# Performance work log

Measured on AMD Instinct MI355X. Metric: run time of the kernel, lower is better.

The kernel has to match this reference:

```python
import jax, jax.numpy as jnp
import numpy as np

ENC_H = 512
DEC_H = 1024

def setup_inputs() -> dict:
    key = jax.random.key(0)
    k1, k2, k3, k4 = jax.random.split(key, 4)
    B, S = 32, 2048
    s = jax.random.normal(k1, (B, DEC_H), dtype=jnp.float32)
    encoder_outputs = jax.random.normal(k2, (B, S, 2 * ENC_H), dtype=jnp.float32)
    # nn.Linear weights: attn: [dec_h, 2*enc_h + dec_h], v: [1, dec_h]
    fan_in_attn = 2 * ENC_H + DEC_H
    attn_w = jax.random.uniform(k3, (DEC_H, fan_in_attn), dtype=jnp.float32,
                                minval=-1.0, maxval=1.0) / np.sqrt(fan_in_attn)
    v_w = jax.random.uniform(k4, (1, DEC_H), dtype=jnp.float32,
                             minval=-1.0, maxval=1.0) / np.sqrt(DEC_H)
    return {"s": s, "encoder_outputs": encoder_outputs, "attn_w": attn_w, "v_w": v_w}

def reference(s, encoder_outputs, attn_w, v_w):
    # Split attn weight to avoid materializing the repeated/concatenated tensor:
    # cat([s_rep, enc], -1) @ W^T == s @ Ws^T (broadcast over S) + enc @ We^T
    W_s = attn_w[:, :DEC_H]            # [dec_h, dec_h] acts on s
    W_e = attn_w[:, DEC_H:]            # [dec_h, 2*enc_h] acts on encoder_outputs
    proj_s = jnp.einsum('bd,hd->bh', s, W_s)                   # [B, dec_h]
    proj_e = jnp.einsum('bse,he->bsh', encoder_outputs, W_e)   # [B, S, dec_h]
    energy = jnp.tanh(proj_s[:, None, :] + proj_e)             # [B, S, dec_h]
    scores = jnp.einsum('bsh,oh->bs', energy, v_w)             # [B, S]
    return jax.nn.softmax(scores, axis=1)
```

## Files before the change

kernel.cpp:

```cpp
#include <hip/hip_runtime.h>
#include <hip/hip_bf16.h>

#define KDIM 1024
#define HDIM 1024
#define BM   64
#define SPART 65536

typedef __attribute__((ext_vector_type(8))) short bf16x8_t;
typedef __attribute__((ext_vector_type(16))) float f32x16_t;
typedef __attribute__((ext_vector_type(4))) float f32x4_t;
typedef __attribute__((ext_vector_type(4))) unsigned int u32x4_t;
typedef __attribute__((ext_vector_type(2))) unsigned int u32x2_t;

#define WAITVM(n) asm volatile("s_waitcnt vmcnt(" #n ")" ::: "memory")
#define MEMFENCE() asm volatile("" ::: "memory")

__device__ __forceinline__ unsigned int pack2bf(float a, float b) {
    union { float f; unsigned int u; } ua, ub;
    ua.f = a; ub.f = b;
    unsigned int ra = (ua.u + 0x7fffu + ((ua.u >> 16) & 1u)) >> 16;
    unsigned int rb = (ub.u + 0x7fffu + ((ub.u >> 16) & 1u)) >> 16;
    return ra | (rb << 16);
}

__device__ __forceinline__ unsigned int cvtpk(float lo, float hi) {
    unsigned int r;
    asm("v_cvt_pk_bf16_f32 %0, %1, %2" : "=v"(r) : "v"(lo), "v"(hi));
    return r;
}

__device__ __forceinline__ void gload16(const void* g, void* l) {
    __builtin_amdgcn_global_load_lds(
        (const __attribute__((address_space(1))) void*)g,
        (__attribute__((address_space(3))) void*)l, 16, 0, 0);
}

__global__ void cvt_we_k(const float* __restrict__ attn_w, unsigned short* __restrict__ we_t) {
    const int h = blockIdx.x;
    const int t = threadIdx.x;
    const f32x4_t v = *(const f32x4_t*)(attn_w + (size_t)h * 2048 + 1024 + (size_t)t * 4);
    u32x2_t o;
    o[0] = pack2bf(v[0], v[1]);
    o[1] = pack2bf(v[2], v[3]);
    const int ks  = t >> 2;
    const int e15 = (t & 3) * 4;
    *(u32x2_t*)&we_t[(size_t)ks * 16384 + h * 16 + e15] = o;
}

__global__ void proj_s_k(const float* __restrict__ s, const float* __restrict__ attn_w,
                         float* __restrict__ ps) {
    const int h = (blockIdx.x * blockDim.x + threadIdx.x) >> 6;
    const int lane = threadIdx.x & 63;
    const float* wr = attn_w + (size_t)h * 2048;
    float w[16];
#pragma unroll
    for (int i = 0; i < 16; ++i) w[i] = wr[lane + 64 * i];
    for (int b = 0; b < 32; ++b) {
        const float* sr = s + (size_t)b * 1024;
        float a = 0.f;
#pragma unroll
        for (int i = 0; i < 16; ++i) a = fmaf(w[i], sr[lane + 64 * i], a);
#pragma unroll
        for (int off = 32; off >= 1; off >>= 1) a += __shfl_xor(a, off, 64);
        if (lane == 0) ps[b * 1024 + h] = a;
    }
}

__launch_bounds__(512, 4)
__global__ void fused_main3_k(const float* __restrict__ enc,
                              const unsigned short* __restrict__ we_t,
                              const float* __restrict__ ps,
                              const float* __restrict__ vw,
                              float* __restrict__ scores_part) {
    __shared__ float lds_a[4 * 64 * 64];

    const int t = threadIdx.x;
    const int bid = blockIdx.x;
    const int xcd   = bid & 7;
    const int hhalf = (bid >> 3) & 1;
    const int m_swz = xcd * 128 + (bid >> 4);
    const int m_base = m_swz * BM;
    const int bidx = m_swz >> 5;

    const int lane = t & 63;
    const int wid  = t >> 6;
    const int l31  = lane & 31;
    const int h5   = lane >> 5;
    const int habs = hhalf * 512 + wid * 64;

    const int gr = t >> 4;
    const int gc = (t & 15) ^ (gr & 15);
    const float* gbase0 = enc + (size_t)(m_base + gr) * KDIM + gc * 4;
    const float* gbase1 = gbase0 + (size_t)32 * KDIM;

    auto stageG = [&](int kc) {
        const float* g0 = gbase0 + kc * 64;
        const float* g1 = gbase1 + kc * 64;
        char* d = (char*)lds_a + (kc & 3) * 16384 + t * 16;
        gload16(g0, d);
        gload16(g1, d + 8192);
    };

    const unsigned short* btile = we_t + (size_t)(habs + l31) * 16 + h5 * 8;
    auto loadB = [&](int g, bf16x8_t* dst) {
        const unsigned short* bp = btile + (size_t)g * 16384;
        dst[0] = *(const bf16x8_t*)(bp);
        dst[1] = *(const bf16x8_t*)(bp + 512);
    };

    f32x16_t acc[2][2];
#pragma unroll
    for (int m = 0; m < 2; ++m)
#pragma unroll
        for (int nf = 0; nf < 2; ++nf)
#pragma unroll
            for (int r = 0; r < 16; ++r) acc[m][nf][r] = 0.f;

    bf16x8_t bbuf[4][2];

    stageG(0);
    stageG(1);
    MEMFENCE();
    loadB(0, bbuf[0]);
    loadB(1, bbuf[1]);
    loadB(2, bbuf[2]);
    WAITVM(8);
    __builtin_amdgcn_s_barrier();
    MEMFENCE();

    const int xr = l31 & 15;
    const int a0base = l31 * 256;
    const int a1base = (32 + l31) * 256;

#pragma unroll
    for (int kc = 0; kc < 16; ++kc) {
        const char* slotp = (const char*)lds_a + (kc & 3) * 16384;
#pragma unroll
        for (int ksl = 0; ksl < 4; ++ksl) {
            const int g = kc * 4 + ksl;
            if (g + 3 < 64) loadB(g + 3, bbuf[(g + 3) & 3]);

            const int co = (((ksl << 2) + (h5 << 1)) ^ xr) << 4;
            const f32x4_t lo0 = *(const f32x4_t*)(slotp + a0base + co);
            const f32x4_t hi0 = *(const f32x4_t*)(slotp + a0base + (co ^ 16));
            const f32x4_t lo1 = *(const f32x4_t*)(slotp + a1base + co);
            const f32x4_t hi1 = *(const f32x4_t*)(slotp + a1base + (co ^ 16));
            union { u32x4_t u; bf16x8_t b; } ca0, ca1;
            ca0.u[0] = cvtpk(lo0[0], lo0[1]);
            ca0.u[1] = cvtpk(lo0[2], lo0[3]);
            ca0.u[2] = cvtpk(hi0[0], hi0[1]);
            ca0.u[3] = cvtpk(hi0[2], hi0[3]);
            ca1.u[0] = cvtpk(lo1[0], lo1[1]);
            ca1.u[1] = cvtpk(lo1[2], lo1[3]);
            ca1.u[2] = cvtpk(hi1[0], hi1[1]);
            ca1.u[3] = cvtpk(hi1[2], hi1[3]);

            const bf16x8_t* bfr = bbuf[g & 3];
            __builtin_amdgcn_s_setprio(1);
            acc[0][0] = __builtin_amdgcn_mfma_f32_32x32x16_bf16(ca0.b, bfr[0], acc[0][0], 0, 0, 0);
            acc[1][0] = __builtin_amdgcn_mfma_f32_32x32x16_bf16(ca1.b, bfr[0], acc[1][0], 0, 0, 0);
            acc[0][1] = __builtin_amdgcn_mfma_f32_32x32x16_bf16(ca0.b, bfr[1], acc[0][1], 0, 0, 0);
            acc[1][1] = __builtin_amdgcn_mfma_f32_32x32x16_bf16(ca1.b, bfr[1], acc[1][1], 0, 0, 0);
            __builtin_amdgcn_s_setprio(0);
        }
        MEMFENCE();
        if (kc + 2 < 16) stageG(kc + 2);
        if (kc < 15) {
            if (kc == 14) WAITVM(8); else WAITVM(10);
            __builtin_amdgcn_s_barrier();
            MEMFENCE();
        }
    }

    float sc2[2][16];
#pragma unroll
    for (int m = 0; m < 2; ++m)
#pragma unroll
        for (int r = 0; r < 16; ++r) sc2[m][r] = 0.f;

#pragma unroll
    for (int nf = 0; nf < 2; ++nf) {
        const int h = habs + nf * 32 + l31;
        const float pv = ps[bidx * 1024 + h];
        const float vv = vw[h];
#pragma unroll
        for (int m = 0; m < 2; ++m)
#pragma unroll
            for (int r = 0; r < 16; ++r) {
                const float x = acc[m][nf][r] + pv;
                const float e = __expf(2.0f * x);
                const float th = 1.0f - __fdividef(2.0f, e + 1.0f);
                sc2[m][r] = fmaf(vv, th, sc2[m][r]);
            }
    }

#pragma unroll
    for (int off = 1; off < 32; off <<= 1)
#pragma unroll
        for (int m = 0; m < 2; ++m)
#pragma unroll
            for (int r = 0; r < 16; ++r)
                sc2[m][r] += __shfl_xor(sc2[m][r], off, 64);

    __syncthreads();
    float* slds = (float*)lds_a;
    if (l31 == 0) {
#pragma unroll
        for (int m = 0; m < 2; ++m)
#pragma unroll
            for (int r = 0; r < 16; ++r) {
                const int row = m * 32 + (r & 3) + 8 * (r >> 2) + 4 * h5;
                slds[wid * 64 + row] = sc2[m][r];
            }
    }
    __syncthreads();
    if (t < 64) {
        float v = 0.f;
#pragma unroll
        for (int w = 0; w < 8; ++w) v += slds[w * 64 + t];
        scores_part[(size_t)hhalf * SPART + m_base + t] = v;
    }
}

__global__ void softmax_k(const float* __restrict__ sc, float* __restrict__ out) {
    const int b = blockIdx.x;
    const int t = threadIdx.x;
    const int lane = t & 63;
    const int w = t >> 6;
    const float* r0 = sc + (size_t)b * 2048;
    const float* r1 = sc + SPART + (size_t)b * 2048;
    float x[8];
#pragma unroll
    for (int i = 0; i < 8; ++i) x[i] = r0[i * 256 + t] + r1[i * 256 + t];
    float m = x[0];
#pragma unroll
    for (int i = 1; i < 8; ++i) m = fmaxf(m, x[i]);
#pragma unroll
    for (int off = 32; off >= 1; off >>= 1) m = fmaxf(m, __shfl_xor(m, off, 64));
    __shared__ float sred[4];
    __shared__ float sred2[4];
    if (lane == 0) sred[w] = m;
    __syncthreads();
    m = fmaxf(fmaxf(sred[0], sred[1]), fmaxf(sred[2], sred[3]));
    float ssum = 0.f;
#pragma unroll
    for (int i = 0; i < 8; ++i) { x[i] = expf(x[i] - m); ssum += x[i]; }
#pragma unroll
    for (int off = 32; off >= 1; off >>= 1) ssum += __shfl_xor(ssum, off, 64);
    if (lane == 0) sred2[w] = ssum;
    __syncthreads();
    const float inv = 1.0f / (sred2[0] + sred2[1] + sred2[2] + sred2[3]);
#pragma unroll
    for (int i = 0; i < 8; ++i) out[(size_t)b * 2048 + i * 256 + t] = x[i] * inv;
}

extern "C" void kernel_launch(void* const* d_in, const int* in_sizes, int n_in,
                              void* d_out, int out_size, void* d_ws, size_t ws_size,
                              hipStream_t stream) {
    const float* s      = (const float*)d_in[0];
    const float* enc    = (const float*)d_in[1];
    const float* attn_w = (const float*)d_in[2];
    const float* vw     = (const float*)d_in[3];
    float* out = (float*)d_out;

    unsigned short* we = (unsigned short*)d_ws;
    float* ps     = (float*)((char*)d_ws + (2u << 20));
    float* scores = (float*)((char*)d_ws + (2u << 20) + (128u << 10));

    cvt_we_k<<<1024, 256, 0, stream>>>(attn_w, we);
    proj_s_k<<<256, 256, 0, stream>>>(s, attn_w, ps);
    fused_main3_k<<<2048, 512, 0, stream>>>(enc, we, ps, vw, scores);
    softmax_k<<<32, 256, 0, stream>>>(scores, out);
}
```

Measured before the change: 269.2 us.

## Enlarge GEMM M-tile to 128 rows with double-buffered LDS staging

The fused projection+tanh+score kernel now processes 128 encoder rows per block instead of 64, giving each wave four M fragments. Each loaded B (weight) fragment is therefore reused across twice as many MFMAs, and half as many blocks are launched. The A-staging pipeline changes from a 4-slot ring with prefetch distance 2 to a 2-slot double buffer with prefetch distance 1. In exchange, accumulator register use doubles (occupancy hint lowered to 2 blocks per CU), and the shallower prefetch may expose more global-load latency.

Result: faster. 229.4 us (-14.8%).

```diff
diff --git a/kernel.cpp b/kernel.cpp
--- a/kernel.cpp
+++ b/kernel.cpp
@@ -3,7 +3,6 @@
 
 #define KDIM 1024
 #define HDIM 1024
-#define BM   64
 #define SPART 65536
 
 typedef __attribute__((ext_vector_type(8))) short bf16x8_t;
@@ -66,21 +65,21 @@
     }
 }
 
-__launch_bounds__(512, 4)
-__global__ void fused_main3_k(const float* __restrict__ enc,
+__launch_bounds__(512, 2)
+__global__ void fused_main4_k(const float* __restrict__ enc,
                               const unsigned short* __restrict__ we_t,
                               const float* __restrict__ ps,
                               const float* __restrict__ vw,
                               float* __restrict__ scores_part) {
-    __shared__ float lds_a[4 * 64 * 64];
+    __shared__ float lds_a[2 * 128 * 64];
 
     const int t = threadIdx.x;
     const int bid = blockIdx.x;
     const int xcd   = bid & 7;
     const int hhalf = (bid >> 3) & 1;
-    const int m_swz = xcd * 128 + (bid >> 4);
-    const int m_base = m_swz * BM;
-    const int bidx = m_swz >> 5;
+    const int m_swz = xcd * 64 + (bid >> 4);
+    const int m_base = m_swz * 128;
+    const int bidx = m_swz >> 4;
 
     const int lane = t & 63;
     const int wid  = t >> 6;
@@ -90,15 +89,15 @@
 
     const int gr = t >> 4;
     const int gc = (t & 15) ^ (gr & 15);
-    const float* gbase0 = enc + (size_t)(m_base + gr) * KDIM + gc * 4;
-    const float* gbase1 = gbase0 + (size_t)32 * KDIM;
+    const float* gb = enc + (size_t)(m_base + gr) * KDIM + gc * 4;
 
     auto stageG = [&](int kc) {
-        const float* g0 = gbase0 + kc * 64;
-        const float* g1 = gbase1 + kc * 64;
-        char* d = (char*)lds_a + (kc & 3) * 16384 + t * 16;
-        gload16(g0, d);
-        gload16(g1, d + 8192);
+        const float* g = gb + kc * 64;
+        char* d = (char*)lds_a + (kc & 1) * 32768 + t * 16;
+        gload16(g,                  d);
+        gload16(g + 32 * KDIM,      d + 8192);
+        gload16(g + 64 * KDIM,      d + 16384);
+        gload16(g + 96 * KDIM,      d + 24576);
     };
 
     const unsigned short* btile = we_t + (size_t)(habs + l31) * 16 + h5 * 8;
@@ -108,9 +107,9 @@
         dst[1] = *(const bf16x8_t*)(bp + 512);
     };
 
-    f32x16_t acc[2][2];
-#pragma unroll
-    for (int m = 0; m < 2; ++m)
+    f32x16_t acc[4][2];
+#pragma unroll
+    for (int m = 0; m < 4; ++m)
 #pragma unroll
         for (int nf = 0; nf < 2; ++nf)
 #pragma unroll
@@ -119,62 +118,55 @@
     bf16x8_t bbuf[4][2];
 
     stageG(0);
-    stageG(1);
     MEMFENCE();
     loadB(0, bbuf[0]);
     loadB(1, bbuf[1]);
     loadB(2, bbuf[2]);
-    WAITVM(8);
+    WAITVM(6);
     __builtin_amdgcn_s_barrier();
-    MEMFENCE();
 
     const int xr = l31 & 15;
-    const int a0base = l31 * 256;
-    const int a1base = (32 + l31) * 256;
 
 #pragma unroll
     for (int kc = 0; kc < 16; ++kc) {
-        const char* slotp = (const char*)lds_a + (kc & 3) * 16384;
+        if (kc + 1 < 16) stageG(kc + 1);
+        MEMFENCE();
+        const char* slotp = (const char*)lds_a + (kc & 1) * 32768;
 #pragma unroll
         for (int ksl = 0; ksl < 4; ++ksl) {
             const int g = kc * 4 + ksl;
             if (g + 3 < 64) loadB(g + 3, bbuf[(g + 3) & 3]);
 
             const int co = (((ksl << 2) + (h5 << 1)) ^ xr) << 4;
-            const f32x4_t lo0 = *(const f32x4_t*)(slotp + a0base + co);
-            const f32x4_t hi0 = *(const f32x4_t*)(slotp + a0base + (co ^ 16));
-            const f32x4_t lo1 = *(const f32x4_t*)(slotp + a1base + co);
-            const f32x4_t hi1 = *(const f32x4_t*)(slotp + a1base + (co ^ 16));
-            union { u32x4_t u; bf16x8_t b; } ca0, ca1;
-            ca0.u[0] = cvtpk(lo0[0], lo0[1]);
-            ca0.u[1] = cvtpk(lo0[2], lo0[3]);
-            ca0.u[2] = cvtpk(hi0[0], hi0[1]);
-            ca0.u[3] = cvtpk(hi0[2], hi0[3]);
-            ca1.u[0] = cvtpk(lo1[0], lo1[1]);
-            ca1.u[1] = cvtpk(lo1[2], lo1[3]);
-            ca1.u[2] = cvtpk(hi1[0], hi1[1]);
-            ca1.u[3] = cvtpk(hi1[2], hi1[3]);
-
+            union { u32x4_t u; bf16x8_t b; } ca[4];
+#pragma unroll
+            for (int mi = 0; mi < 4; ++mi) {
+                const char* rowp = slotp + mi * 8192 + l31 * 256;
+                const f32x4_t lo = *(const f32x4_t*)(rowp + co);
+                const f32x4_t hi = *(const f32x4_t*)(rowp + (co ^ 16));
+                ca[mi].u[0] = cvtpk(lo[0], lo[1]);
+                ca[mi].u[1] = cvtpk(lo[2], lo[3]);
+                ca[mi].u[2] = cvtpk(hi[0], hi[1]);
+                ca[mi].u[3] = cvtpk(hi[2], hi[3]);
+            }
             const bf16x8_t* bfr = bbuf[g & 3];
             __builtin_amdgcn_s_setprio(1);
-            acc[0][0] = __builtin_amdgcn_mfma_f32_32x32x16_bf16(ca0.b, bfr[0], acc[0][0], 0, 0, 0);
-            acc[1][0] = __builtin_amdgcn_mfma_f32_32x32x16_bf16(ca1.b, bfr[0], acc[1][0], 0, 0, 0);
-            acc[0][1] = __builtin_amdgcn_mfma_f32_32x32x16_bf16(ca0.b, bfr[1], acc[0][1], 0, 0, 0);
-            acc[1][1] = __builtin_amdgcn_mfma_f32_32x32x16_bf16(ca1.b, bfr[1], acc[1][1], 0, 0, 0);
+#pragma unroll
+            for (int mi = 0; mi < 4; ++mi) {
+                acc[mi][0] = __builtin_amdgcn_mfma_f32_32x32x16_bf16(ca[mi].b, bfr[0], acc[mi][0], 0, 0, 0);
+                acc[mi][1] = __builtin_amdgcn_mfma_f32_32x32x16_bf16(ca[mi].b, bfr[1], acc[mi][1], 0, 0, 0);
+            }
             __builtin_amdgcn_s_setprio(0);
         }
-        MEMFENCE();
-        if (kc + 2 < 16) stageG(kc + 2);
-        if (kc < 15) {
-            if (kc == 14) WAITVM(8); else WAITVM(10);
+        if (kc + 1 < 16) {
+            WAITVM(6);
             __builtin_amdgcn_s_barrier();
-            MEMFENCE();
         }
     }
 
-    float sc2[2][16];
-#pragma unroll
-    for (int m = 0; m < 2; ++m)
+    float sc2[4][16];
+#pragma unroll
+    for (int m = 0; m < 4; ++m)
 #pragma unroll
         for (int r = 0; r < 16; ++r) sc2[m][r] = 0.f;
 
@@ -184,7 +176,7 @@
         const float pv = ps[bidx * 1024 + h];
         const float vv = vw[h];
 #pragma unroll
-        for (int m = 0; m < 2; ++m)
+        for (int m = 0; m < 4; ++m)
 #pragma unroll
             for (int r = 0; r < 16; ++r) {
                 const float x = acc[m][nf][r] + pv;
@@ -197,7 +189,7 @@
 #pragma unroll
     for (int off = 1; off < 32; off <<= 1)
 #pragma unroll
-        for (int m = 0; m < 2; ++m)
+        for (int m = 0; m < 4; ++m)
 #pragma unroll
             for (int r = 0; r < 16; ++r)
                 sc2[m][r] += __shfl_xor(sc2[m][r], off, 64);
@@ -206,18 +198,18 @@
     float* slds = (float*)lds_a;
     if (l31 == 0) {
 #pragma unroll
-        for (int m = 0; m < 2; ++m)
+        for (int m = 0; m < 4; ++m)
 #pragma unroll
             for (int r = 0; r < 16; ++r) {
                 const int row = m * 32 + (r & 3) + 8 * (r >> 2) + 4 * h5;
-                slds[wid * 64 + row] = sc2[m][r];
-            }
-    }
-    __syncthreads();
-    if (t < 64) {
+                slds[wid * 128 + row] = sc2[m][r];
+            }
+    }
+    __syncthreads();
+    if (t < 128) {
         float v = 0.f;
 #pragma unroll
-        for (int w = 0; w < 8; ++w) v += slds[w * 64 + t];
+        for (int w = 0; w < 8; ++w) v += slds[w * 128 + t];
         scores_part[(size_t)hhalf * SPART + m_base + t] = v;
     }
 }
@@ -269,6 +261,6 @@
 
     cvt_we_k<<<1024, 256, 0, stream>>>(attn_w, we);
     proj_s_k<<<256, 256, 0, stream>>>(s, attn_w, ps);
-    fused_main3_k<<<2048, 512, 0, stream>>>(enc, we, ps, vw, scores);
+    fused_main4_k<<<1024, 512, 0, stream>>>(enc, we, ps, vw, scores);
     softmax_k<<<32, 256, 0, stream>>>(scores, out);
 }
```
